# Performance work log

Hardware: AMD Instinct MI355X
Metric: run time of the kernel (lower is better)

Reference implementation:

```python
import jax, jax.numpy as jnp
import numpy as np

B, S, MV = 32, 64, 30
V, E, H, L = 20000, 256, 512, 128
PAD_IDX = 0
THETA = 0.5


def setup_inputs() -> dict:
    key = jax.random.key(0)
    ks = jax.random.split(key, 12)
    sc = 0.02
    return {
        "z": jax.random.normal(ks[0], (B, L), jnp.float32),
        "input_sequence": jax.random.randint(ks[1], (B, S, MV), 0, V),
        "length": jax.random.randint(ks[2], (B,), 1, S + 1),
        "embedding_weight": jax.random.normal(ks[3], (V, E), jnp.float32) * sc,
        "W_l2h": jax.random.normal(ks[4], (H, L), jnp.float32) * sc,
        "b_l2h": jax.random.normal(ks[5], (H,), jnp.float32) * sc,
        "W_ih": jax.random.normal(ks[6], (3 * H, E), jnp.float32) * sc,
        "W_hh": jax.random.normal(ks[7], (3 * H, H), jnp.float32) * sc,
        "b_ih": jax.random.normal(ks[8], (3 * H,), jnp.float32) * sc,
        "b_hh": jax.random.normal(ks[9], (3 * H,), jnp.float32) * sc,
        "W_out": jax.random.normal(ks[10], (V, H), jnp.float32) * sc,
        "b_out": jax.random.normal(ks[11], (V,), jnp.float32) * sc,
    }


def _gru(emb, h0, W_ih, W_hh, b_ih, b_hh):
    # emb: (B,S,E); PyTorch GRU cell, single layer.
    def step(h, x_t):
        gi = x_t @ W_ih.T + b_ih          # (B,3H)
        gh = h @ W_hh.T + b_hh            # (B,3H)
        i_r, i_z, i_n = jnp.split(gi, 3, axis=-1)
        h_r, h_z, h_n = jnp.split(gh, 3, axis=-1)
        r = jax.nn.sigmoid(i_r + h_r)
        zt = jax.nn.sigmoid(i_z + h_z)
        n = jnp.tanh(i_n + r * h_n)
        h_new = (1.0 - zt) * n + zt * h
        return h_new, h_new
    _, outs = jax.lax.scan(step, h0, jnp.swapaxes(emb, 0, 1))  # (S,B,H)
    return jnp.swapaxes(outs, 0, 1)  # (B,S,H)


def reference(z, input_sequence, length, embedding_weight, W_l2h, b_l2h,
              W_ih, W_hh, b_ih, b_hh, W_out, b_out):
    # Multi-hot scatter: zeros.scatter_(2, idx, 1)
    mh = jnp.zeros((B, S, V), jnp.float32).at[
        jnp.arange(B)[:, None, None], jnp.arange(S)[None, :, None], input_sequence
    ].set(1.0)
    mh = mh.at[:, :, PAD_IDX].set(0.0)
    # Dense one-hot matmul embedding-sum (faithful to torch.mm on (B*S,V))
    emb = jnp.tanh(jnp.einsum('bsv,ve->bse', mh, embedding_weight))
    h0 = z @ W_l2h.T + b_l2h                      # (B,H)
    outputs = _gru(emb, h0, W_ih, W_hh, b_ih, b_hh)  # (B,S,H)
    # pack/pad semantics: outputs beyond each length are zero
    valid = jnp.arange(S)[None, :] < length[:, None]
    outputs = outputs * valid[..., None]
    m_output = jnp.sum(jnp.abs(outputs), axis=2) > 0  # (B,S) bool
    logits = jnp.einsum('bsh,vh->bsv', outputs, W_out) + b_out  # (B,S,V)
    p_output = jax.nn.sigmoid(logits)
    # _sample: top-k over logits[..., 3:], shift by 3, threshold via sigmoid
    top_p, top_i = jax.lax.top_k(logits[..., 3:], MV)
    top_i = top_i + 3
    s_output = jnp.where(jax.nn.sigmoid(top_p) <= THETA, PAD_IDX, top_i)  # (B,S,MV)
    return (p_output, s_output, m_output)
```

## Files before the change

kernel.cpp:

```cpp
#include <hip/hip_runtime.h>
#include <hip/hip_bf16.h>
#include <math.h>

#define B_ 32
#define S_ 64
#define MV_ 30
#define V_ 20000
#define E_ 256
#define H_ 512
#define L_ 128
#define H3_ 1536
#define BS_ 2048
#define NB4 256
#define NEG7 -3.0e38f
#define SENT 0xFFF8000000000000ULL

typedef __attribute__((ext_vector_type(8))) short short8v;
typedef __attribute__((ext_vector_type(4))) float f32x4;
typedef unsigned long long ull_;

__global__ __launch_bounds__(256) void k12(const int* __restrict__ seq,
                                           const float* __restrict__ Ew,
                                           const float* __restrict__ z,
                                           const float* __restrict__ Wl,
                                           const float* __restrict__ bl,
                                           double* __restrict__ emb,
                                           double* __restrict__ hstep) {
    __shared__ int sidx[MV_];
    int bid = blockIdx.x;
    int t = threadIdx.x;
    if (bid < BS_) {
        int row = bid;
        if (t < MV_) sidx[t] = seq[row * MV_ + t];
        __syncthreads();
        double acc = 0.0;
        for (int i = 0; i < MV_; ++i) {
            int id = sidx[i];
            if (id == 0) continue;
            bool dup = false;
            for (int q = 0; q < i; ++q) dup = dup || (sidx[q] == id);
            if (!dup) acc += (double)Ew[(size_t)id * E_ + t];
        }
        emb[(size_t)row * E_ + t] = tanh(acc);
    } else if (bid < BS_ + 64) {
        int o = (bid - BS_) * 256 + t;
        int b = o >> 9;
        int j = o & 511;
        const float4* zr = (const float4*)(z + (size_t)b * L_);
        const float4* wr = (const float4*)(Wl + (size_t)j * L_);
        double acc = (double)bl[j];
#pragma unroll
        for (int k = 0; k < L_ / 4; ++k) {
            float4 a = zr[k];
            float4 w = wr[k];
            acc += (double)a.x * (double)w.x + (double)a.y * (double)w.y
                 + (double)a.z * (double)w.z + (double)a.w * (double)w.w;
        }
        hstep[(size_t)(b >> 2) * 2048 + j * 4 + (b & 3)] = acc;
    } else {
        ull_* hs = (ull_*)hstep;
        size_t i = (size_t)(bid - (BS_ + 64)) * 1024 + (size_t)t * 4;
        hs[16384 + i + 0] = SENT;
        hs[16384 + i + 1] = SENT;
        hs[16384 + i + 2] = SENT;
        hs[16384 + i + 3] = SENT;
    }
}

__global__ __launch_bounds__(256) void k3_gi(const double* __restrict__ A,
                                             const float* __restrict__ Bm,
                                             const float* __restrict__ bih,
                                             double* __restrict__ gi) {
    __shared__ double As[16][66];
    __shared__ double Bs[16][66];
    int t = threadIdx.x;
    int n0 = blockIdx.x * 64;
    int m0 = blockIdx.y * 64;
    int tx = t & 15, ty = t >> 4;
    int ml = t >> 2;
    int kl = (t & 3) * 4;
    double acc[4][4];
#pragma unroll
    for (int i = 0; i < 4; ++i)
#pragma unroll
        for (int j = 0; j < 4; ++j) acc[i][j] = 0.0;

    for (int kt = 0; kt < 256; kt += 16) {
        double4 av = *(const double4*)(A + (size_t)(m0 + ml) * 256 + kt + kl);
        float4 bv = *(const float4*)(Bm + (size_t)(n0 + ml) * 256 + kt + kl);
        As[kl + 0][ml] = av.x; As[kl + 1][ml] = av.y; As[kl + 2][ml] = av.z; As[kl + 3][ml] = av.w;
        Bs[kl + 0][ml] = (double)bv.x; Bs[kl + 1][ml] = (double)bv.y;
        Bs[kl + 2][ml] = (double)bv.z; Bs[kl + 3][ml] = (double)bv.w;
        __syncthreads();
#pragma unroll
        for (int kk = 0; kk < 16; ++kk) {
            double2 a01 = *(const double2*)&As[kk][ty * 4];
            double2 a23 = *(const double2*)&As[kk][ty * 4 + 2];
            double2 b01 = *(const double2*)&Bs[kk][tx * 4];
            double2 b23 = *(const double2*)&Bs[kk][tx * 4 + 2];
            double am[4] = {a01.x, a01.y, a23.x, a23.y};
            double bn[4] = {b01.x, b01.y, b23.x, b23.y};
#pragma unroll
            for (int i = 0; i < 4; ++i)
#pragma unroll
                for (int j = 0; j < 4; ++j) acc[i][j] += am[i] * bn[j];
        }
        __syncthreads();
    }
#pragma unroll
    for (int i = 0; i < 4; ++i) {
        int m = m0 + ty * 4 + i;
        int bb = m >> 6, ss = m & 63;
#pragma unroll
        for (int j = 0; j < 4; ++j) {
            int n = n0 + tx * 4 + j;
            int g = n >> 9, u = n & 511;
            gi[(((size_t)(ss * 512 + u)) * 3 + g) * 32 + bb] = acc[i][j] + (double)bih[n];
        }
    }
}

__global__ __launch_bounds__(256, 1) void k4_gru(const double* __restrict__ gi,
                                                 const float* __restrict__ whh,
                                                 const float* __restrict__ bhh,
                                                 const int* __restrict__ length,
                                                 double* __restrict__ hstep,
                                                 float* __restrict__ outs) {
    __shared__ double hl[2112];
    __shared__ double part[2][4][16][13];

    int t = threadIdx.x;
    int wv = t >> 6;
    int lane = t & 63;
    int bid = blockIdx.x;
    int g = bid & 7;
    int beta = bid >> 3;

    int ul = lane >> 2, ks = lane & 3;

    const float* wbase = whh + ((size_t)(beta * 16 + ul)) * 512 + wv * 128 + ks * 32;
    float4 w0r[8], w1r[8], w2r[8];
#pragma unroll
    for (int c = 0; c < 8; ++c) {
        w0r[c] = *(const float4*)(wbase + c * 4);
        w1r[c] = *(const float4*)(wbase + 512 * 512 + c * 4);
        w2r[c] = *(const float4*)(wbase + 1024 * 512 + c * 4);
    }

    const double* hg0 = hstep + (size_t)g * 2048;
    {
#pragma unroll
        for (int j = 0; j < 8; ++j) {
            int e = t + j * 256;
            hl[e + ((e >> 7) << 2)] = hg0[e];
        }
    }
    __syncthreads();

    int u2 = lane >> 2, b2 = lane & 3;
    int u_g = beta * 16 + u2;
    int b_g = g * 4 + b2;
    double gr = 0.0, gz = 0.0, gn = 0.0, bhr_ = 0.0, bhz_ = 0.0, bhn_ = 0.0;
    double hv = 0.0;
    int len = 0;
    if (wv == 0) {
        bhr_ = (double)bhh[u_g];
        bhz_ = (double)bhh[u_g + 512];
        bhn_ = (double)bhh[u_g + 1024];
        len = length[b_g];
        hv = hg0[u_g * 4 + b2];
        size_t gb = ((size_t)u_g * 3) * 32 + b_g;
        gr = gi[gb]; gz = gi[gb + 32]; gn = gi[gb + 64];
    }

    const double* hr = &hl[(wv * 128 + ks * 32) * 4 + ((wv * 4 + ks) << 2)];
    int sbase = ks * 128 + ul * 4;

    for (int s = 0; s < S_; ++s) {
        int par = s & 1;
        ull_ ta[4], tb[4];
        const ull_* src = (const ull_*)(hstep + (size_t)s * 16384 + (size_t)g * 2048)
                          + wv * 512;
        if (s > 0) {
            while (true) {
                bool ok = true;
#pragma unroll
                for (int j = 0; j < 4; ++j) {
                    ta[j] = __hip_atomic_load(&src[sbase + j], __ATOMIC_RELAXED,
                                              __HIP_MEMORY_SCOPE_AGENT);
                    ok = ok && (ta[j] != SENT);
                }
                if (__all(ok)) break;
                __builtin_amdgcn_s_sleep(1);
            }
#pragma unroll
            for (int j = 0; j < 4; ++j)
                tb[j] = __hip_atomic_load(&src[sbase + 64 + j], __ATOMIC_RELAXED,
                                          __HIP_MEMORY_SCOPE_AGENT);
            asm volatile("" ::: "memory");
            {
                ull_* hlu = (ull_*)hl;
#pragma unroll
                for (int j = 0; j < 4; ++j) {
                    int e = wv * 512 + sbase + j;
                    hlu[e + ((e >> 7) << 2)] = ta[j];
                }
            }
        }

        double a0[4] = {0, 0, 0, 0}, a1[4] = {0, 0, 0, 0}, a2[4] = {0, 0, 0, 0};
#pragma unroll
        for (int c = 0; c < 4; ++c) {
            const double* hp = hr + c * 16;
            double2 hA0 = *(const double2*)(hp + 0),  hB0 = *(const double2*)(hp + 2);
            double2 hA1 = *(const double2*)(hp + 4),  hB1 = *(const double2*)(hp + 6);
            double2 hA2 = *(const double2*)(hp + 8),  hB2 = *(const double2*)(hp + 10);
            double2 hA3 = *(const double2*)(hp + 12), hB3 = *(const double2*)(hp + 14);
            float4 w0 = w0r[c], w1 = w1r[c], w2 = w2r[c];
            { double d0 = (double)w0.x, d1 = (double)w1.x, d2 = (double)w2.x;
              a0[0] += hA0.x * d0; a0[1] += hA0.y * d0; a0[2] += hB0.x * d0; a0[3] += hB0.y * d0;
              a1[0] += hA0.x * d1; a1[1] += hA0.y * d1; a1[2] += hB0.x * d1; a1[3] += hB0.y * d1;
              a2[0] += hA0.x * d2; a2[1] += hA0.y * d2; a2[2] += hB0.x * d2; a2[3] += hB0.y * d2; }
            { double d0 = (double)w0.y, d1 = (double)w1.y, d2 = (double)w2.y;
              a0[0] += hA1.x * d0; a0[1] += hA1.y * d0; a0[2] += hB1.x * d0; a0[3] += hB1.y * d0;
              a1[0] += hA1.x * d1; a1[1] += hA1.y * d1; a1[2] += hB1.x * d1; a1[3] += hB1.y * d1;
              a2[0] += hA1.x * d2; a2[1] += hA1.y * d2; a2[2] += hB1.x * d2; a2[3] += hB1.y * d2; }
            { double d0 = (double)w0.z, d1 = (double)w1.z, d2 = (double)w2.z;
              a0[0] += hA2.x * d0; a0[1] += hA2.y * d0; a0[2] += hB2.x * d0; a0[3] += hB2.y * d0;
              a1[0] += hA2.x * d1; a1[1] += hA2.y * d1; a1[2] += hB2.x * d1; a1[3] += hB2.y * d1;
              a2[0] += hA2.x * d2; a2[1] += hA2.y * d2; a2[2] += hB2.x * d2; a2[3] += hB2.y * d2; }
            { double d0 = (double)w0.w, d1 = (double)w1.w, d2 = (double)w2.w;
              a0[0] += hA3.x * d0; a0[1] += hA3.y * d0; a0[2] += hB3.x * d0; a0[3] += hB3.y * d0;
              a1[0] += hA3.x * d1; a1[1] += hA3.y * d1; a1[2] += hB3.x * d1; a1[3] += hB3.y * d1;
              a2[0] += hA3.x * d2; a2[1] += hA3.y * d2; a2[2] += hB3.x * d2; a2[3] += hB3.y * d2; }
        }

        if (s > 0) {
            while (true) {
                bool ok = true;
#pragma unroll
                for (int j = 0; j < 4; ++j) ok = ok && (tb[j] != SENT);
                if (__all(ok)) break;
                __builtin_amdgcn_s_sleep(1);
#pragma unroll
                for (int j = 0; j < 4; ++j)
                    tb[j] = __hip_atomic_load(&src[sbase + 64 + j], __ATOMIC_RELAXED,
                                              __HIP_MEMORY_SCOPE_AGENT);
            }
            asm volatile("" ::: "memory");
            {
                ull_* hlu = (ull_*)hl;
#pragma unroll
                for (int j = 0; j < 4; ++j) {
                    int e = wv * 512 + sbase + 64 + j;
                    hlu[e + ((e >> 7) << 2)] = tb[j];
                }
            }
        }

#pragma unroll
        for (int c = 4; c < 8; ++c) {
            const double* hp = hr + c * 16;
            double2 hA0 = *(const double2*)(hp + 0),  hB0 = *(const double2*)(hp + 2);
            double2 hA1 = *(const double2*)(hp + 4),  hB1 = *(const double2*)(hp + 6);
            double2 hA2 = *(const double2*)(hp + 8),  hB2 = *(const double2*)(hp + 10);
            double2 hA3 = *(const double2*)(hp + 12), hB3 = *(const double2*)(hp + 14);
            float4 w0 = w0r[c], w1 = w1r[c], w2 = w2r[c];
            { double d0 = (double)w0.x, d1 = (double)w1.x, d2 = (double)w2.x;
              a0[0] += hA0.x * d0; a0[1] += hA0.y * d0; a0[2] += hB0.x * d0; a0[3] += hB0.y * d0;
              a1[0] += hA0.x * d1; a1[1] += hA0.y * d1; a1[2] += hB0.x * d1; a1[3] += hB0.y * d1;
              a2[0] += hA0.x * d2; a2[1] += hA0.y * d2; a2[2] += hB0.x * d2; a2[3] += hB0.y * d2; }
            { double d0 = (double)w0.y, d1 = (double)w1.y, d2 = (double)w2.y;
              a0[0] += hA1.x * d0; a0[1] += hA1.y * d0; a0[2] += hB1.x * d0; a0[3] += hB1.y * d0;
              a1[0] += hA1.x * d1; a1[1] += hA1.y * d1; a1[2] += hB1.x * d1; a1[3] += hB1.y * d1;
              a2[0] += hA1.x * d2; a2[1] += hA1.y * d2; a2[2] += hB1.x * d2; a2[3] += hB1.y * d2; }
            { double d0 = (double)w0.z, d1 = (double)w1.z, d2 = (double)w2.z;
              a0[0] += hA2.x * d0; a0[1] += hA2.y * d0; a0[2] += hB2.x * d0; a0[3] += hB2.y * d0;
              a1[0] += hA2.x * d1; a1[1] += hA2.y * d1; a1[2] += hB2.x * d1; a1[3] += hB2.y * d1;
              a2[0] += hA2.x * d2; a2[1] += hA2.y * d2; a2[2] += hB2.x * d2; a2[3] += hB2.y * d2; }
            { double d0 = (double)w0.w, d1 = (double)w1.w, d2 = (double)w2.w;
              a0[0] += hA3.x * d0; a0[1] += hA3.y * d0; a0[2] += hB3.x * d0; a0[3] += hB3.y * d0;
              a1[0] += hA3.x * d1; a1[1] += hA3.y * d1; a1[2] += hB3.x * d1; a1[3] += hB3.y * d1;
              a2[0] += hA3.x * d2; a2[1] += hA3.y * d2; a2[2] += hB3.x * d2; a2[3] += hB3.y * d2; }
        }

#pragma unroll
        for (int b = 0; b < 4; ++b) {
            a0[b] += __shfl_xor(a0[b], 1); a0[b] += __shfl_xor(a0[b], 2);
            a1[b] += __shfl_xor(a1[b], 1); a1[b] += __shfl_xor(a1[b], 2);
            a2[b] += __shfl_xor(a2[b], 1); a2[b] += __shfl_xor(a2[b], 2);
        }
        if (ks == 0) {
#pragma unroll
            for (int b = 0; b < 4; ++b) {
                part[par][wv][ul][0 * 4 + b] = a0[b];
                part[par][wv][ul][1 * 4 + b] = a1[b];
                part[par][wv][ul][2 * 4 + b] = a2[b];
            }
        }
        __syncthreads();

        if (wv == 0) {
            double s0 = part[par][0][u2][0 * 4 + b2] + part[par][1][u2][0 * 4 + b2]
                      + part[par][2][u2][0 * 4 + b2] + part[par][3][u2][0 * 4 + b2];
            double s1 = part[par][0][u2][1 * 4 + b2] + part[par][1][u2][1 * 4 + b2]
                      + part[par][2][u2][1 * 4 + b2] + part[par][3][u2][1 * 4 + b2];
            double s2 = part[par][0][u2][2 * 4 + b2] + part[par][1][u2][2 * 4 + b2]
                      + part[par][2][u2][2 * 4 + b2] + part[par][3][u2][2 * 4 + b2];
            double r  = 1.0 / (1.0 + exp(-(gr + s0 + bhr_)));
            double zt = 1.0 / (1.0 + exp(-(gz + s1 + bhz_)));
            double n  = tanh(gn + r * (s2 + bhn_));
            double hn_ = (1.0 - zt) * n + zt * hv;
            hv = hn_;
            if (s < S_ - 1) {
                ull_* hdst = (ull_*)(hstep + (size_t)(s + 1) * 16384 + (size_t)g * 2048);
                __hip_atomic_store(&hdst[beta * 64 + lane],
                                   __builtin_bit_cast(ull_, hn_),
                                   __ATOMIC_RELAXED, __HIP_MEMORY_SCOPE_AGENT);
                size_t gb = ((size_t)((s + 1) * 512 + u_g) * 3) * 32 + b_g;
                gr = gi[gb]; gz = gi[gb + 32]; gn = gi[gb + 64];
            }
            outs[(size_t)(b_g * 64 + s) * H_ + u_g] = (s < len) ? (float)hn_ : 0.0f;
        }
    }
}

__device__ __forceinline__ unsigned short f2b_(float x) {
    unsigned u = __builtin_bit_cast(unsigned, x);
    return (unsigned short)((u + 0x7FFFu + ((u >> 16) & 1u)) >> 16);
}
__device__ __forceinline__ short8v pack8_(float4 a, float4 b) {
    short8v r;
    r[0] = (short)f2b_(a.x); r[1] = (short)f2b_(a.y);
    r[2] = (short)f2b_(a.z); r[3] = (short)f2b_(a.w);
    r[4] = (short)f2b_(b.x); r[5] = (short)f2b_(b.y);
    r[6] = (short)f2b_(b.z); r[7] = (short)f2b_(b.w);
    return r;
}
__global__ __launch_bounds__(256) void k_prep2(const float* __restrict__ Wsrc,
                                               const float* __restrict__ Asrc,
                                               short* __restrict__ W16,
                                               short* __restrict__ A16) {
    int bid = blockIdx.x, t = threadIdx.x;
    if (bid < 5000) {
        int i = bid * 256 + t;
        float4 a = *(const float4*)&Wsrc[(size_t)i * 8];
        float4 b = *(const float4*)&Wsrc[(size_t)i * 8 + 4];
        *(short8v*)&W16[(size_t)i * 8] = pack8_(a, b);
    } else {
        int i = (bid - 5000) * 256 + t;
        float4 a = *(const float4*)&Asrc[(size_t)i * 8];
        float4 b = *(const float4*)&Asrc[(size_t)i * 8 + 4];
        *(short8v*)&A16[(size_t)i * 8] = pack8_(a, b);
    }
}

#define LDK5 72
__global__ __launch_bounds__(256, 2) void k5_mfma(const short* __restrict__ A16,
                                                  const short* __restrict__ W16,
                                                  const float* __restrict__ bo,
                                                  float* __restrict__ pOut) {
    __shared__ short As[128 * LDK5];
    __shared__ short Bs[128 * LDK5];
    int t = threadIdx.x;
    int bid = blockIdx.x;
    int swz = (bid & 7) * 314 + (bid >> 3);
    int m0 = (swz & 15) * 128;
    int n0 = (swz >> 4) * 128;
    int lane = t & 63, wv = t >> 6;
    int wr = wv >> 1, wc = wv & 1;
    int ml = t >> 1;
    int kl = (t & 1) * 32;

    const short* Arow = A16 + (size_t)(m0 + ml) * H_ + kl;
    int vrow = n0 + ml;
    bool vok = vrow < V_;
    const short* Wrow = W16 + (size_t)(vok ? vrow : 0) * H_ + kl;
    short8v zz = (short8v){0, 0, 0, 0, 0, 0, 0, 0};

    f32x4 acc[4][4];
#pragma unroll
    for (int i = 0; i < 4; ++i)
#pragma unroll
        for (int j = 0; j < 4; ++j) acc[i][j] = (f32x4){0.f, 0.f, 0.f, 0.f};

    int ko = lane >> 4;
    int rr = lane & 15;

    for (int kt = 0; kt < H_; kt += 64) {
        short8v a0 = *(const short8v*)(Arow + kt);
        short8v a1 = *(const short8v*)(Arow + kt + 8);
        short8v a2 = *(const short8v*)(Arow + kt + 16);
        short8v a3 = *(const short8v*)(Arow + kt + 24);
        short8v b0 = vok ? *(const short8v*)(Wrow + kt) : zz;
        short8v b1 = vok ? *(const short8v*)(Wrow + kt + 8) : zz;
        short8v b2 = vok ? *(const short8v*)(Wrow + kt + 16) : zz;
        short8v b3 = vok ? *(const short8v*)(Wrow + kt + 24) : zz;
        *(short8v*)&As[ml * LDK5 + kl]      = a0;
        *(short8v*)&As[ml * LDK5 + kl + 8]  = a1;
        *(short8v*)&As[ml * LDK5 + kl + 16] = a2;
        *(short8v*)&As[ml * LDK5 + kl + 24] = a3;
        *(short8v*)&Bs[ml * LDK5 + kl]      = b0;
        *(short8v*)&Bs[ml * LDK5 + kl + 8]  = b1;
        *(short8v*)&Bs[ml * LDK5 + kl + 16] = b2;
        *(short8v*)&Bs[ml * LDK5 + kl + 24] = b3;
        __syncthreads();

#pragma unroll
        for (int kh = 0; kh < 2; ++kh) {
            short8v af[4], bf[4];
#pragma unroll
            for (int i = 0; i < 4; ++i)
                af[i] = *(const short8v*)&As[(wr * 64 + i * 16 + rr) * LDK5 + kh * 32 + ko * 8];
#pragma unroll
            for (int j = 0; j < 4; ++j)
                bf[j] = *(const short8v*)&Bs[(wc * 64 + j * 16 + rr) * LDK5 + kh * 32 + ko * 8];
#pragma unroll
            for (int i = 0; i < 4; ++i)
#pragma unroll
                for (int j = 0; j < 4; ++j)
                    acc[i][j] = __builtin_amdgcn_mfma_f32_16x16x32_bf16(af[i], bf[j], acc[i][j], 0, 0, 0);
        }
        __syncthreads();
    }

    int cr4 = (lane >> 4) * 4;
    float bov[4];
#pragma unroll
    for (int j = 0; j < 4; ++j) {
        int v = n0 + wc * 64 + j * 16 + rr;
        bov[j] = (v < V_) ? bo[v] : 0.f;
    }
#pragma unroll
    for (int i = 0; i < 4; ++i) {
#pragma unroll
        for (int j = 0; j < 4; ++j) {
            int v = n0 + wc * 64 + j * 16 + rr;
            if (v < V_) {
#pragma unroll
                for (int r = 0; r < 4; ++r) {
                    int m = m0 + wr * 64 + i * 16 + cr4 + r;
                    float x = acc[i][j][r] + bov[j];
                    pOut[(size_t)m * V_ + v] = 1.0f / (1.0f + expf(-x));
                }
            }
        }
    }
}

__global__ __launch_bounds__(512) void k7a_cand(const float* __restrict__ pOut,
                                                float* __restrict__ candV,
                                                int* __restrict__ candI) {
    int row = blockIdx.x;
    int t = threadIdx.x;
    int wv = t >> 6;
    int lane = t & 63;
    const float* rowp = pOut + (size_t)row * V_ + wv * 2500;

    float rv[40];
#pragma unroll
    for (int q4 = 0; q4 < 10; ++q4) {
        int base = q4 * 256 + lane * 4;
        float4 v4 = *(const float4*)(rowp + base);
        float vv[4] = {v4.x, v4.y, v4.z, v4.w};
#pragma unroll
        for (int c = 0; c < 4; ++c) {
            int li = base + c;
            int col = wv * 2500 + li;
            bool ok = (li < 2500) && (col >= 3);
            rv[q4 * 4 + c] = ok ? vv[c] : NEG7;
        }
    }
    float m1 = rv[0]; int s1 = 0;
#pragma unroll
    for (int q = 1; q < 40; ++q)
        if (rv[q] > m1) { m1 = rv[q]; s1 = q; }
    float m2 = NEG7; int s2 = 0;
#pragma unroll
    for (int q = 0; q < 40; ++q)
        if (q != s1 && rv[q] > m2) { m2 = rv[q]; s2 = q; }
    bool dirty = false;
    ull_ used = 0;
    int myidx = wv * 2500 + (s1 >> 2) * 256 + lane * 4 + (s1 & 3);

    float keepv = NEG7; int keepi = 0;
#pragma unroll 1
    for (int r = 0; r < 32; ++r) {
        float bv = m1; int bi = myidx;
#pragma unroll
        for (int m = 1; m < 64; m <<= 1) {
            float ov = __shfl_xor(bv, m);
            int   oi = __shfl_xor(bi, m);
            if (ov > bv || (ov == bv && oi < bi)) { bv = ov; bi = oi; }
        }
        if (lane == r) { keepv = bv; keepi = bi; }
        if (myidx == bi) {
            used |= (1ull << s1);
            if (!dirty) {
                m1 = m2; s1 = s2; dirty = true;
            } else {
                m1 = NEG7; s1 = 0;
#pragma unroll
                for (int q = 0; q < 40; ++q) {
                    float v = ((used >> q) & 1ull) ? NEG7 : rv[q];
                    if (v > m1) { m1 = v; s1 = q; }
                }
                m2 = NEG7; s2 = 0;
#pragma unroll
                for (int q = 0; q < 40; ++q) {
                    float v = (((used >> q) & 1ull) || q == s1) ? NEG7 : rv[q];
                    if (v > m2) { m2 = v; s2 = q; }
                }
                dirty = false;
            }
            myidx = wv * 2500 + (s1 >> 2) * 256 + lane * 4 + (s1 & 3);
        }
    }
    if (lane < 32) {
        size_t o = ((size_t)row * 8 + wv) * 32 + lane;
        candV[o] = keepv;
        candI[o] = keepi;
    }
}

__global__ __launch_bounds__(256) void k7b_final(const float* __restrict__ candV,
                                                 const int* __restrict__ candI,
                                                 const float* __restrict__ outs,
                                                 const float* __restrict__ W,
                                                 const float* __restrict__ bo,
                                                 float* __restrict__ mOut,
                                                 float* __restrict__ sOut) {
    __shared__ float selv[64];
    __shared__ int   seli[64];
    __shared__ float resv[64];
    __shared__ float redm[4];
    __shared__ __align__(16) float orow[H_];

    int row = blockIdx.x;
    int t = threadIdx.x;
    int lane = t & 63, wid = t >> 6;

    if (wid != 0) {
        for (int i = t - 64; i < H_; i += 192)
            orow[i] = outs[(size_t)row * H_ + i];
    } else {
        float cv[4]; int ci[4];
#pragma unroll
        for (int q = 0; q < 4; ++q) {
            size_t o = (size_t)row * 256 + q * 64 + lane;
            cv[q] = candV[o];
            ci[q] = candI[o];
        }
        float lv = cv[0]; int lix = ci[0]; int ls = 0;
#pragma unroll
        for (int q = 1; q < 4; ++q)
            if (cv[q] > lv || (cv[q] == lv && ci[q] < lix)) { lv = cv[q]; lix = ci[q]; ls = q; }

#pragma unroll 1
        for (int r = 0; r < 64; ++r) {
            float bv = lv; int bi = lix;
#pragma unroll
            for (int m = 1; m < 64; m <<= 1) {
                float ov = __shfl_xor(bv, m);
                int   oi = __shfl_xor(bi, m);
                if (ov > bv || (ov == bv && oi < bi)) { bv = ov; bi = oi; }
            }
            if (lane == r) { selv[r] = bv; seli[r] = bi; }
            if (lix == bi) {
#pragma unroll
                for (int q = 0; q < 4; ++q) cv[q] = (ls == q) ? NEG7 : cv[q];
                lv = cv[0]; lix = ci[0]; ls = 0;
#pragma unroll
                for (int q = 1; q < 4; ++q)
                    if (cv[q] > lv || (cv[q] == lv && ci[q] < lix)) { lv = cv[q]; lix = ci[q]; ls = q; }
            }
        }
    }
    __syncthreads();

    {
        float ms = fabsf(orow[t]) + fabsf(orow[t + 256]);
#pragma unroll
        for (int m = 1; m < 64; m <<= 1) ms += __shfl_xor(ms, m);
        if (lane == 0) redm[wid] = ms;
    }

    {
        int c = t >> 2, q = t & 3;
        int gidx = seli[c];
        const float4* w4 = (const float4*)(W + (size_t)gidx * H_);
        const float4* o4 = (const float4*)orow;
        double acc = 0.0;
#pragma unroll 8
        for (int i2 = 0; i2 < 32; ++i2) {
            float4 wv4 = w4[i2 * 4 + q];
            float4 ov4 = o4[i2 * 4 + q];
            acc += (double)wv4.x * (double)ov4.x + (double)wv4.y * (double)ov4.y
                 + (double)wv4.z * (double)ov4.z + (double)wv4.w * (double)ov4.w;
        }
        acc += __shfl_xor(acc, 1);
        acc += __shfl_xor(acc, 2);
        if (q == 0) resv[c] = (float)(acc + (double)bo[gidx]);
    }
    __syncthreads();

    if (t == 0)
        mOut[row] = (redm[0] + redm[1] + redm[2] + redm[3] > 0.f) ? 1.f : 0.f;

    if (t < 64) {
        float v = resv[t];
        int idx = seli[t];
#pragma unroll 1
        for (int r = 0; r < MV_; ++r) {
            float bv = v; int bi = idx;
#pragma unroll
            for (int m = 1; m < 64; m <<= 1) {
                float ov = __shfl_xor(bv, m);
                int   oi = __shfl_xor(bi, m);
                if (ov > bv || (ov == bv && oi < bi)) { bv = ov; bi = oi; }
            }
            if (t == 0)
                sOut[(size_t)row * MV_ + r] = (bv <= 0.0f) ? 0.0f : (float)bi;
            if (idx == bi) v = NEG7;
        }
    }
}

extern "C" void kernel_launch(void* const* d_in, const int* in_sizes, int n_in,
                              void* d_out, int out_size, void* d_ws, size_t ws_size,
                              hipStream_t stream) {
    const float* z      = (const float*)d_in[0];
    const int*   seq    = (const int*)d_in[1];
    const int*   length = (const int*)d_in[2];
    const float* Ew     = (const float*)d_in[3];
    const float* W_l2h  = (const float*)d_in[4];
    const float* b_l2h  = (const float*)d_in[5];
    const float* W_ih   = (const float*)d_in[6];
    const float* W_hh   = (const float*)d_in[7];
    const float* b_ih   = (const float*)d_in[8];
    const float* b_hh   = (const float*)d_in[9];
    const float* W_out  = (const float*)d_in[10];
    const float* b_out  = (const float*)d_in[11];

    float* out = (float*)d_out;

    double* emb_d = (double*)d_ws;
    double* gi_d  = emb_d + 524288;
    double* hstep = gi_d + 3145728;
    float*  outs  = (float*)(hstep + 1048576);
    float*  candV = outs + 1048576;
    int*    candI = (int*)(candV + (size_t)BS_ * 256);
    short*  A16   = (short*)emb_d;
    short*  W16   = (short*)gi_d;

    float* pOut = out;
    float* sOut = out + (size_t)BS_ * V_;
    float* mOut = sOut + (size_t)BS_ * MV_;

    k12<<<BS_ + 64 + 1008, 256, 0, stream>>>(seq, Ew, z, W_l2h, b_l2h, emb_d, hstep);
    k3_gi<<<dim3(24, 32), 256, 0, stream>>>(emb_d, W_ih, b_ih, gi_d);
    k4_gru<<<NB4, 256, 0, stream>>>(gi_d, W_hh, b_hh, length, hstep, outs);
    k_prep2<<<5512, 256, 0, stream>>>(W_out, outs, W16, A16);
    k5_mfma<<<2512, 256, 0, stream>>>(A16, W16, b_out, pOut);
    k7a_cand<<<BS_, 512, 0, stream>>>(pOut, candV, candI);
    k7b_final<<<BS_, 256, 0, stream>>>(candV, candI, outs, W_out, b_out, mOut, sOut);
}
```

Baseline: 697.5 us.

## Coalesce GRU hidden-state polling loads and emit bf16 outputs directly from GRU

The GRU kernel now reads the published hidden state with lane-contiguous addresses (stride-64 chunks per lane) instead of 4 consecutive elements per lane, so the spin-wait atomic loads are coalesced. It also writes the bf16-rounded output alongside the fp32 output, which removes the activation-conversion half of the prep kernel. The prep kernel now only converts W_out. The cost is extra scattered 2-byte stores inside the serial GRU loop, which sits on the critical path.

```diff
diff --git a/kernel.cpp b/kernel.cpp
--- a/kernel.cpp
+++ b/kernel.cpp
@@ -125,7 +125,8 @@
                                                  const float* __restrict__ bhh,
                                                  const int* __restrict__ length,
                                                  double* __restrict__ hstep,
-                                                 float* __restrict__ outs) {
+                                                 float* __restrict__ outs,
+                                                 short* __restrict__ A16) {
     __shared__ double hl[2112];
     __shared__ double part[2][4][16][13];
 
@@ -174,7 +175,6 @@
     }
 
     const double* hr = &hl[(wv * 128 + ks * 32) * 4 + ((wv * 4 + ks) << 2)];
-    int sbase = ks * 128 + ul * 4;
 
     for (int s = 0; s < S_; ++s) {
         int par = s & 1;
@@ -186,8 +186,8 @@
                 bool ok = true;
 #pragma unroll
                 for (int j = 0; j < 4; ++j) {
-                    ta[j] = __hip_atomic_load(&src[sbase + j], __ATOMIC_RELAXED,
-                                              __HIP_MEMORY_SCOPE_AGENT);
+                    ta[j] = __hip_atomic_load(&src[(2 * j) * 64 + lane],
+                                              __ATOMIC_RELAXED, __HIP_MEMORY_SCOPE_AGENT);
                     ok = ok && (ta[j] != SENT);
                 }
                 if (__all(ok)) break;
@@ -195,14 +195,14 @@
             }
 #pragma unroll
             for (int j = 0; j < 4; ++j)
-                tb[j] = __hip_atomic_load(&src[sbase + 64 + j], __ATOMIC_RELAXED,
-                                          __HIP_MEMORY_SCOPE_AGENT);
+                tb[j] = __hip_atomic_load(&src[(2 * j + 1) * 64 + lane],
+                                          __ATOMIC_RELAXED, __HIP_MEMORY_SCOPE_AGENT);
             asm volatile("" ::: "memory");
             {
                 ull_* hlu = (ull_*)hl;
 #pragma unroll
                 for (int j = 0; j < 4; ++j) {
-                    int e = wv * 512 + sbase + j;
+                    int e = wv * 512 + (2 * j) * 64 + lane;
                     hlu[e + ((e >> 7) << 2)] = ta[j];
                 }
             }
@@ -244,15 +244,15 @@
                 __builtin_amdgcn_s_sleep(1);
 #pragma unroll
                 for (int j = 0; j < 4; ++j)
-                    tb[j] = __hip_atomic_load(&src[sbase + 64 + j], __ATOMIC_RELAXED,
-                                              __HIP_MEMORY_SCOPE_AGENT);
+                    tb[j] = __hip_atomic_load(&src[(2 * j + 1) * 64 + lane],
+                                              __ATOMIC_RELAXED, __HIP_MEMORY_SCOPE_AGENT);
             }
             asm volatile("" ::: "memory");
             {
                 ull_* hlu = (ull_*)hl;
 #pragma unroll
                 for (int j = 0; j < 4; ++j) {
-                    int e = wv * 512 + sbase + 64 + j;
+                    int e = wv * 512 + (2 * j + 1) * 64 + lane;
                     hlu[e + ((e >> 7) << 2)] = tb[j];
                 }
             }
@@ -320,7 +320,13 @@
                 size_t gb = ((size_t)((s + 1) * 512 + u_g) * 3) * 32 + b_g;
                 gr = gi[gb]; gz = gi[gb + 32]; gn = gi[gb + 64];
             }
-            outs[(size_t)(b_g * 64 + s) * H_ + u_g] = (s < len) ? (float)hn_ : 0.0f;
+            float ov = (s < len) ? (float)hn_ : 0.0f;
+            size_t oidx = (size_t)(b_g * 64 + s) * H_ + u_g;
+            outs[oidx] = ov;
+            {
+                unsigned u = __builtin_bit_cast(unsigned, ov);
+                A16[oidx] = (short)((u + 0x7FFFu + ((u >> 16) & 1u)) >> 16);
+            }
         }
     }
 }
@@ -338,21 +344,11 @@
     return r;
 }
 __global__ __launch_bounds__(256) void k_prep2(const float* __restrict__ Wsrc,
-                                               const float* __restrict__ Asrc,
-                                               short* __restrict__ W16,
-                                               short* __restrict__ A16) {
-    int bid = blockIdx.x, t = threadIdx.x;
-    if (bid < 5000) {
-        int i = bid * 256 + t;
-        float4 a = *(const float4*)&Wsrc[(size_t)i * 8];
-        float4 b = *(const float4*)&Wsrc[(size_t)i * 8 + 4];
-        *(short8v*)&W16[(size_t)i * 8] = pack8_(a, b);
-    } else {
-        int i = (bid - 5000) * 256 + t;
-        float4 a = *(const float4*)&Asrc[(size_t)i * 8];
-        float4 b = *(const float4*)&Asrc[(size_t)i * 8 + 4];
-        *(short8v*)&A16[(size_t)i * 8] = pack8_(a, b);
-    }
+                                               short* __restrict__ W16) {
+    int i = blockIdx.x * 256 + threadIdx.x;
+    float4 a = *(const float4*)&Wsrc[(size_t)i * 8];
+    float4 b = *(const float4*)&Wsrc[(size_t)i * 8 + 4];
+    *(short8v*)&W16[(size_t)i * 8] = pack8_(a, b);
 }
 
 #define LDK5 72
@@ -659,8 +655,8 @@
 
     k12<<<BS_ + 64 + 1008, 256, 0, stream>>>(seq, Ew, z, W_l2h, b_l2h, emb_d, hstep);
     k3_gi<<<dim3(24, 32), 256, 0, stream>>>(emb_d, W_ih, b_ih, gi_d);
-    k4_gru<<<NB4, 256, 0, stream>>>(gi_d, W_hh, b_hh, length, hstep, outs);
-    k_prep2<<<5512, 256, 0, stream>>>(W_out, outs, W16, A16);
+    k4_gru<<<NB4, 256, 0, stream>>>(gi_d, W_hh, b_hh, length, hstep, outs, A16);
+    k_prep2<<<5000, 256, 0, stream>>>(W_out, W16);
     k5_mfma<<<2512, 256, 0, stream>>>(A16, W16, b_out, pOut);
     k7a_cand<<<BS_, 512, 0, stream>>>(pOut, candV, candI);
     k7b_final<<<BS_, 256, 0, stream>>>(candV, candI, outs, W_out, b_out, mOut, sOut);
```

Result: faster. 659.7 us (median of 2 runs) (-5.4%).
